# Kernel optimization log

Measured on AMD Instinct MI355X. Metric: run time of the kernel, lower is better.

Reference implementation:

```python
import jax, jax.numpy as jnp
import numpy as np
import math

B, TQ, TK, C, H, DFF = 4, 1024, 1024, 1024, 16, 4096
DK = C // H
EPS = 1e-12


def _mha(x_q, x_kv, wq, bq, wk, bk, wv, bv, wo, bo, mask):
    Bq, Tq, Cq = x_q.shape
    Tk = x_kv.shape[1]
    q = (x_q @ wq + bq).reshape(Bq, Tq, H, DK).transpose(0, 2, 1, 3)  # [B,H,Tq,dk]
    k = (x_kv @ wk + bk).reshape(Bq, Tk, H, DK).transpose(0, 2, 1, 3)
    v = (x_kv @ wv + bv).reshape(Bq, Tk, H, DK).transpose(0, 2, 1, 3)
    scores = jnp.einsum('bhqd,bhkd->bhqk', q, k) * (1.0 / math.sqrt(DK))
    if mask is not None:
        scores = jnp.where(mask, scores, jnp.asarray(-1e9, scores.dtype))
    attn = jax.nn.softmax(scores, axis=-1)
    o = jnp.einsum('bhqk,bhkd->bhqd', attn, v).transpose(0, 2, 1, 3).reshape(Bq, Tq, Cq)
    return o @ wo + bo


def _ln(x, g, b):
    mu = jnp.mean(x, axis=-1, keepdims=True)
    var = jnp.mean(jnp.square(x - mu), axis=-1, keepdims=True)
    return (x - mu) * jax.lax.rsqrt(var + EPS) * g + b


def setup_inputs() -> dict:
    key = jax.random.key(0)
    ks = iter(jax.random.split(key, 32))
    s = 0.02
    inp = {}
    inp['src'] = jax.random.normal(next(ks), (B, TK, C), jnp.float32)
    inp['dst'] = jax.random.normal(next(ks), (B, TQ, C), jnp.float32)
    inp['src_mask'] = jnp.ones((B, 1, 1, TK), dtype=bool)  # key-padding mask (all valid)
    inp['dst_mask'] = jnp.tril(jnp.ones((TQ, TQ), dtype=bool))[None, None]  # causal
    for p in ['sa', 'ca']:
        for n in ['wq', 'wk', 'wv', 'wo']:
            inp[f'{p}_{n}'] = jax.random.normal(next(ks), (C, C), jnp.float32) * s
        for n in ['bq', 'bk', 'bv', 'bo']:
            inp[f'{p}_{n}'] = jnp.zeros((C,), jnp.float32)
    inp['ffn_w1'] = jax.random.normal(next(ks), (C, DFF), jnp.float32) * s
    inp['ffn_b1'] = jnp.zeros((DFF,), jnp.float32)
    inp['ffn_w2'] = jax.random.normal(next(ks), (DFF, C), jnp.float32) * s
    inp['ffn_b2'] = jnp.zeros((C,), jnp.float32)
    for i in ['1', '2', '3']:
        inp[f'ln{i}_g'] = jnp.ones((C,), jnp.float32)
        inp[f'ln{i}_b'] = jnp.zeros((C,), jnp.float32)
    return inp


def reference(src, dst, src_mask, dst_mask,
              sa_wq, sa_wk, sa_wv, sa_wo, sa_bq, sa_bk, sa_bv, sa_bo,
              ca_wq, ca_wk, ca_wv, ca_wo, ca_bq, ca_bk, ca_bv, ca_bo,
              ffn_w1, ffn_b1, ffn_w2, ffn_b2,
              ln1_g, ln1_b, ln2_g, ln2_b, ln3_g, ln3_b):
    # post-LN decoder layer, eval mode (dropout is identity)
    sa = _mha(dst, dst, sa_wq, sa_bq, sa_wk, sa_bk, sa_wv, sa_bv, sa_wo, sa_bo, dst_mask)
    y = _ln(dst + sa, ln1_g, ln1_b)
    ca = _mha(y, src, ca_wq, ca_bq, ca_wk, ca_bk, ca_wv, ca_bv, ca_wo, ca_bo, src_mask)
    y = _ln(y + ca, ln2_g, ln2_b)
    ff = jax.nn.gelu(y @ ffn_w1 + ffn_b1, approximate=False) @ ffn_w2 + ffn_b2
    return _ln(y + ff, ln3_g, ln3_b)
```

## Files before the change

### kernel.cpp

```cpp
#include <hip/hip_runtime.h>
#include <math.h>

typedef __attribute__((ext_vector_type(4))) float f32x4;
typedef __attribute__((ext_vector_type(8))) __bf16 bf16x8;
typedef __attribute__((ext_vector_type(8))) short short8;

#define DEV __device__ __forceinline__

DEV short f2bfs(float f) {
    unsigned u = __builtin_bit_cast(unsigned, f);
    unsigned r = (u + 0x7FFFu + ((u >> 16) & 1u)) >> 16;
    return (short)r;
}

DEV f32x4 mfma16(bf16x8 a, bf16x8 b, f32x4 c) {
    return __builtin_amdgcn_mfma_f32_16x16x32_bf16(a, b, c, 0, 0, 0);
}

DEV void gload_lds16(const void* g, void* l) {
    __builtin_amdgcn_global_load_lds((const __attribute__((address_space(1))) void*)g,
                                     (__attribute__((address_space(3))) void*)l, 16, 0, 0);
}

__global__ __launch_bounds__(256) void wtrans(const float* __restrict__ Win,
                                              short* __restrict__ Wout,
                                              int Kd, int Nd) {
    __shared__ float Tt[32][33];
    const int tx = threadIdx.x & 31, ty = threadIdx.x >> 5;
    const int k0 = blockIdx.y * 32, n0 = blockIdx.x * 32;
#pragma unroll
    for (int rr = 0; rr < 4; ++rr) {
        int k = ty * 4 + rr;
        Tt[k][tx] = Win[(size_t)(k0 + k) * Nd + n0 + tx];
    }
    __syncthreads();
#pragma unroll
    for (int rr = 0; rr < 4; ++rr) {
        int n = ty * 4 + rr;
        Wout[(size_t)(n0 + n) * Kd + k0 + tx] = f2bfs(Tt[tx][n]);
    }
}

struct WPtrs { const float* p[8]; };

__global__ __launch_bounds__(256) void wtrans8(WPtrs wp, short* __restrict__ out) {
    const float* __restrict__ Win = wp.p[blockIdx.z];
    short* __restrict__ Wout = out + (size_t)blockIdx.z * (1024 * 1024);
    __shared__ float Tt[32][33];
    const int tx = threadIdx.x & 31, ty = threadIdx.x >> 5;
    const int k0 = blockIdx.y * 32, n0 = blockIdx.x * 32;
#pragma unroll
    for (int rr = 0; rr < 4; ++rr) {
        int k = ty * 4 + rr;
        Tt[k][tx] = Win[(size_t)(k0 + k) * 1024 + n0 + tx];
    }
    __syncthreads();
#pragma unroll
    for (int rr = 0; rr < 4; ++rr) {
        int n = ty * 4 + rr;
        Wout[(size_t)(n0 + n) * 1024 + k0 + tx] = f2bfs(Tt[tx][n]);
    }
}

__global__ __launch_bounds__(256) void conv_bf16(const float* __restrict__ X,
                                                 short* __restrict__ Y, int n4) {
    int i = blockIdx.x * 256 + threadIdx.x;
    if (i < n4) {
        float4 v = ((const float4*)X)[i];
        short4 o;
        o.x = f2bfs(v.x); o.y = f2bfs(v.y); o.z = f2bfs(v.z); o.w = f2bfs(v.w);
        ((short4*)Y)[i] = o;
    }
}

template <int BM, int BN, int EPI, bool SWZ>
__global__ __launch_bounds__(256, (BM == 64 && BN == 64) ? 8 : 1)
void gemm_bt(const short* __restrict__ A,
             const short* __restrict__ BT,
             const float* __restrict__ b0,
             const float* __restrict__ b1,
             const float* __restrict__ b2,
             void* __restrict__ o0,
             void* __restrict__ o1,
             void* __restrict__ o2,
             int M, int N, int K, int Ks) {
    constexpr int IM = BM / 32, JN = BN / 32;
    constexpr int AL = (BM * 64) / 4096;
    constexpr int BL = (BN * 64) / 4096;
    __shared__ __align__(16) short As[2][BM * 32];
    __shared__ __align__(16) short Bs[2][128 * 32];
    const int tid = threadIdx.x, lane = tid & 63, w = tid >> 6;

    int bx, by, bz;
    if (SWZ) {
        int gx = gridDim.x, gy = gridDim.y;
        int G = gx * gy * gridDim.z;
        int fid = blockIdx.x + gx * (blockIdx.y + gy * blockIdx.z);
        int nf = (fid & 7) * (G >> 3) + (fid >> 3);
        bx = nf % gx;
        int t = nf / gx;
        by = t % gy;
        bz = t / gy;
    } else {
        bx = blockIdx.x; by = blockIdx.y; bz = blockIdx.z;
    }

    const int m0 = by * BM, n0 = bx * BN;
    const int kz = bz * K;
    const int wm = (w & 1) * (BM / 2), wn = (w >> 1) * (BN / 2);
    const int rl = lane & 15, rg = lane >> 4;
    f32x4 acc[IM][JN] = {};
    const char* Ab = (const char*)A;
    const char* Bb = (const char*)BT;
    const int nk = K >> 5;

    auto stage = [&](int kt, int buf) {
#pragma unroll
        for (int r = 0; r < AL; ++r) {
            int lo = (tid + r * 256) * 16;
            int row = lo >> 6, cp = (lo >> 4) & 3, c = (cp - (row >> 1)) & 3;
            gload_lds16(Ab + ((size_t)(m0 + row) * Ks + kz + kt * 32 + c * 8) * 2,
                        (char*)As[buf] + lo);
        }
#pragma unroll
        for (int r = 0; r < BL; ++r) {
            int lo = (tid + r * 256) * 16;
            int row = lo >> 6, cp = (lo >> 4) & 3, c = (cp - (row >> 1)) & 3;
            gload_lds16(Bb + ((size_t)(n0 + row) * Ks + kz + kt * 32 + c * 8) * 2,
                        (char*)Bs[buf] + lo);
        }
    };

    stage(0, 0);
    for (int kt = 0; kt < nk; ++kt) {
        const int buf = kt & 1;
        __syncthreads();
        if (kt + 1 < nk) stage(kt + 1, buf ^ 1);
        bf16x8 af[IM], bfr[JN];
#pragma unroll
        for (int i = 0; i < IM; i++) {
            int row = wm + i * 16 + rl;
            af[i] = *(const bf16x8*)(As[buf] + row * 32 + ((rg + (row >> 1)) & 3) * 8);
        }
#pragma unroll
        for (int j = 0; j < JN; j++) {
            int row = wn + j * 16 + rl;
            bfr[j] = *(const bf16x8*)(Bs[buf] + row * 32 + ((rg + (row >> 1)) & 3) * 8);
        }
#pragma unroll
        for (int i = 0; i < IM; i++)
#pragma unroll
            for (int j = 0; j < JN; j++)
                acc[i][j] = mfma16(af[i], bfr[j], acc[i][j]);
    }

    float* o0z = (float*)o0 + (size_t)bz * M * N;
#pragma unroll
    for (int i = 0; i < IM; i++) {
        int gm0 = m0 + wm + i * 16 + rg * 4;
#pragma unroll
        for (int j = 0; j < JN; j++) {
            int gn = n0 + wn + j * 16 + rl;
            if (EPI == 0) {
                float bv = bz == 0 ? b0[gn] : 0.0f;
#pragma unroll
                for (int r = 0; r < 4; r++)
                    o0z[(size_t)(gm0 + r) * N + gn] = acc[i][j][r] + bv;
            } else if (EPI == 2) {
                float bv = b0[gn];
#pragma unroll
                for (int r = 0; r < 4; r++) {
                    float x = acc[i][j][r] + bv;
                    float z = 1.59576912f * x + 0.07135481f * x * x * x;
                    float g = x / (1.0f + __expf(-z));
                    ((short*)o0)[(size_t)(gm0 + r) * N + gn] = f2bfs(g);
                }
            } else {
                int seg = gn >> 10, n1 = gn & 1023, h = n1 >> 6, d = n1 & 63;
                int b = gm0 >> 10, t0 = gm0 & 1023;
                bool isV = (EPI == 1) ? (seg == 2) : (seg == 1);
                const float* bp = (EPI == 1) ? (seg == 0 ? b0 : (seg == 1 ? b1 : b2))
                                             : (seg == 0 ? b0 : b1);
                float bv = bp[n1];
                float qs = (EPI == 1 && seg == 0) ? 0.125f : 1.0f;
                if (!isV) {
                    short* hp = (short*)((EPI == 1) ? (seg == 0 ? o0 : o1) : o0);
                    size_t base = ((size_t)(b * 16 + h) * 1024 + t0) * 64 + d;
#pragma unroll
                    for (int r = 0; r < 4; r++)
                        hp[base + (size_t)r * 64] = f2bfs((acc[i][j][r] + bv) * qs);
                } else {
                    short* vp = (short*)((EPI == 1) ? o2 : o1);
                    short4 pk;
                    pk.x = f2bfs(acc[i][j][0] + bv);
                    pk.y = f2bfs(acc[i][j][1] + bv);
                    pk.z = f2bfs(acc[i][j][2] + bv);
                    pk.w = f2bfs(acc[i][j][3] + bv);
                    *(short4*)(vp + ((size_t)(b * 16 + h) * 64 + d) * 1024 + t0) = pk;
                }
            }
        }
    }
}

template <bool CAUSAL>
__global__ __launch_bounds__(256, 3) void attn4(const short* __restrict__ Qh,
                                                const short* __restrict__ Kh,
                                                const short* __restrict__ VTh,
                                                short* __restrict__ Out, int TKn) {
    __shared__ __align__(16) short Ks[2][64 * 64];
    __shared__ __align__(16) short Vts[2][64 * 64];
    __shared__ __align__(16) short Ps[4][16 * 72 + 8];
    const int tid = threadIdx.x, lane = tid & 63, w = tid >> 6;
    const int rl = lane & 15, rg = lane >> 4;
    const int bh = blockIdx.y, b = bh >> 4, h = bh & 15;
    const int q0 = blockIdx.x * 64;
    const short* Qp = Qh + (size_t)bh * 1024 * 64;
    const char* Kp = (const char*)(Kh + (size_t)bh * (size_t)TKn * 64);
    const char* Vp = (const char*)(VTh + (size_t)bh * (size_t)TKn * 64);

    const int qrow = q0 + w * 16 + rl;
    const bf16x8 qf0 = *(const bf16x8*)(Qp + (size_t)qrow * 64 + rg * 8);
    const bf16x8 qf1 = *(const bf16x8*)(Qp + (size_t)qrow * 64 + 32 + rg * 8);

    bf16x8 onesf;
#pragma unroll
    for (int i = 0; i < 8; ++i) onesf[i] = (__bf16)1.0f;

    f32x4 o[4] = {};
    f32x4 lacc = {};

    short* Pw = &Ps[w][0];
    const int nkt = CAUSAL ? blockIdx.x + 1 : (TKn >> 6);

    auto stage = [&](int kt, int buf) {
#pragma unroll
        for (int r = 0; r < 2; ++r) {
            int lo = (w * 2 + r) * 1024 + lane * 16;
            int row = lo >> 7, cp = (lo >> 4) & 7, c = (cp - row) & 7;
            gload_lds16(Kp + ((size_t)(kt * 64 + row) * 64 + c * 8) * 2,
                        (char*)Ks[buf] + lo);
            gload_lds16(Vp + ((size_t)row * TKn + kt * 64 + c * 8) * 2,
                        (char*)Vts[buf] + lo);
        }
    };

    stage(0, 0);
    for (int kt = 0; kt < nkt; ++kt) {
        const int buf = kt & 1;
        __syncthreads();
        if (kt + 1 < nkt) stage(kt + 1, buf ^ 1);

        const short* KsB = Ks[buf];
        f32x4 s[4];
#pragma unroll
        for (int ch = 0; ch < 4; ++ch) {
            int row = ch * 16 + rl;
            bf16x8 k0 = *(const bf16x8*)(KsB + row * 64 + ((rg + row) & 7) * 8);
            bf16x8 k1 = *(const bf16x8*)(KsB + row * 64 + ((rg + 4 + row) & 7) * 8);
            f32x4 z = {};
            z = mfma16(k0, qf0, z);
            z = mfma16(k1, qf1, z);
            s[ch] = z;
        }
        const bool domask = CAUSAL && (kt == nkt - 1);
#pragma unroll
        for (int ch = 0; ch < 4; ++ch) {
            float p[4];
#pragma unroll
            for (int r = 0; r < 4; ++r) {
                float e = __expf(s[ch][r]);
                if (domask) {
                    int key = kt * 64 + ch * 16 + rg * 4 + r;
                    if (key > qrow) e = 0.0f;
                }
                p[r] = e;
            }
            unsigned d0 = (__builtin_bit_cast(unsigned, p[1]) & 0xFFFF0000u) |
                          (__builtin_bit_cast(unsigned, p[0]) >> 16);
            unsigned d1 = (__builtin_bit_cast(unsigned, p[3]) & 0xFFFF0000u) |
                          (__builtin_bit_cast(unsigned, p[2]) >> 16);
            uint2 dv; dv.x = d0; dv.y = d1;
            *(uint2*)(Pw + rl * 72 + ch * 16 + rg * 4) = dv;
        }
        bf16x8 pa0 = *(const bf16x8*)(Pw + rl * 72 + rg * 8);
        bf16x8 pa1 = *(const bf16x8*)(Pw + rl * 72 + 32 + rg * 8);
        lacc = mfma16(pa0, onesf, lacc);
        lacc = mfma16(pa1, onesf, lacc);
        const short* VsB = Vts[buf];
#pragma unroll
        for (int j = 0; j < 4; ++j) {
            int row = j * 16 + rl;
            bf16x8 v0 = *(const bf16x8*)(VsB + row * 64 + ((rg + row) & 7) * 8);
            bf16x8 v1 = *(const bf16x8*)(VsB + row * 64 + ((rg + 4 + row) & 7) * 8);
            o[j] = mfma16(pa0, v0, o[j]);
            o[j] = mfma16(pa1, v1, o[j]);
        }
    }

    float inv[4];
#pragma unroll
    for (int r = 0; r < 4; r++) inv[r] = 1.0f / lacc[r];
#pragma unroll
    for (int j = 0; j < 4; j++) {
#pragma unroll
        for (int r = 0; r < 4; r++) {
            int row = q0 + w * 16 + rg * 4 + r;
            int col = h * 64 + j * 16 + rl;
            Out[((size_t)b * 1024 + row) * 1024 + col] = f2bfs(o[j][r] * inv[r]);
        }
    }
}

__global__ __launch_bounds__(256) void ln_fused(const float* __restrict__ X,
                                                const float* __restrict__ R,
                                                const float* __restrict__ R2,
                                                const float* __restrict__ gam,
                                                const float* __restrict__ bet,
                                                float* __restrict__ Yf,
                                                short* __restrict__ Yb) {
    const int row = blockIdx.x, tid = threadIdx.x;
    const int lane = tid & 63, w = tid >> 6;
    float4 xv = ((const float4*)(X + (size_t)row * 1024))[tid];
    float4 rv = ((const float4*)(R + (size_t)row * 1024))[tid];
    float v0 = xv.x + rv.x, v1 = xv.y + rv.y, v2 = xv.z + rv.z, v3 = xv.w + rv.w;
    if (R2) {
        float4 r2 = ((const float4*)(R2 + (size_t)row * 1024))[tid];
        v0 += r2.x; v1 += r2.y; v2 += r2.z; v3 += r2.w;
    }
    float s = v0 + v1 + v2 + v3;
    float ss = v0 * v0 + v1 * v1 + v2 * v2 + v3 * v3;
#pragma unroll
    for (int off = 1; off < 64; off <<= 1) {
        s += __shfl_xor(s, off);
        ss += __shfl_xor(ss, off);
    }
    __shared__ float sred[4], ssred[4];
    if (lane == 0) { sred[w] = s; ssred[w] = ss; }
    __syncthreads();
    s = sred[0] + sred[1] + sred[2] + sred[3];
    ss = ssred[0] + ssred[1] + ssred[2] + ssred[3];
    float mu = s * (1.0f / 1024.0f);
    float var = ss * (1.0f / 1024.0f) - mu * mu;
    float rsq = rsqrtf(var + 1e-12f);
    float4 gv = ((const float4*)gam)[tid];
    float4 bv = ((const float4*)bet)[tid];
    float y0 = (v0 - mu) * rsq * gv.x + bv.x;
    float y1 = (v1 - mu) * rsq * gv.y + bv.y;
    float y2 = (v2 - mu) * rsq * gv.z + bv.z;
    float y3 = (v3 - mu) * rsq * gv.w + bv.w;
    float4 yo = {y0, y1, y2, y3};
    ((float4*)(Yf + (size_t)row * 1024))[tid] = yo;
    if (Yb) {
        short4 ob;
        ob.x = f2bfs(y0); ob.y = f2bfs(y1); ob.z = f2bfs(y2); ob.w = f2bfs(y3);
        ((short4*)(Yb + (size_t)row * 1024))[tid] = ob;
    }
}

extern "C" void kernel_launch(void* const* d_in, const int* in_sizes, int n_in,
                              void* d_out, int out_size, void* d_ws, size_t ws_size,
                              hipStream_t stream) {
    const float* src = (const float*)d_in[0];
    const float* dst = (const float*)d_in[1];
    const float* sa_wq = (const float*)d_in[4];
    const float* sa_wk = (const float*)d_in[5];
    const float* sa_wv = (const float*)d_in[6];
    const float* sa_wo = (const float*)d_in[7];
    const float* sa_bq = (const float*)d_in[8];
    const float* sa_bk = (const float*)d_in[9];
    const float* sa_bv = (const float*)d_in[10];
    const float* sa_bo = (const float*)d_in[11];
    const float* ca_wq = (const float*)d_in[12];
    const float* ca_wk = (const float*)d_in[13];
    const float* ca_wv = (const float*)d_in[14];
    const float* ca_wo = (const float*)d_in[15];
    const float* ca_bq = (const float*)d_in[16];
    const float* ca_bk = (const float*)d_in[17];
    const float* ca_bv = (const float*)d_in[18];
    const float* ca_bo = (const float*)d_in[19];
    const float* ffn_w1 = (const float*)d_in[20];
    const float* ffn_b1 = (const float*)d_in[21];
    const float* ffn_w2 = (const float*)d_in[22];
    const float* ffn_b2 = (const float*)d_in[23];
    const float* ln1g = (const float*)d_in[24];
    const float* ln1b = (const float*)d_in[25];
    const float* ln2g = (const float*)d_in[26];
    const float* ln2b = (const float*)d_in[27];
    const float* ln3g = (const float*)d_in[28];
    const float* ln3b = (const float*)d_in[29];

    char* ws = (char*)d_ws;
    size_t off = 0;
    auto alloc = [&](size_t n) { size_t o = off; off = (off + n + 255) & ~(size_t)255; return o; };

    const size_t szW = (size_t)1024 * 1024 * 2;
    short* wT = (short*)(ws + alloc(8 * szW));
    short* w1T = (short*)(ws + alloc((size_t)4096 * 1024 * 2));
    short* w2T = (short*)(ws + alloc((size_t)1024 * 4096 * 2));
    const size_t szAct2 = (size_t)4096 * 1024 * 2;
    const size_t szAct4 = (size_t)4096 * 1024 * 4;
    short* dstb = (short*)(ws + alloc(szAct2));
    short* srcb = (short*)(ws + alloc(szAct2));
    short* Qh = (short*)(ws + alloc(szAct2));
    short* Kh = (short*)(ws + alloc(szAct2));
    short* VTh = (short*)(ws + alloc(szAct2));
    short* attnb = (short*)(ws + alloc(szAct2));
    float* tmp = (float*)(ws + alloc(2 * szAct4));
    float* tmp2 = tmp + (size_t)4096 * 1024;
    float* y1f = (float*)(ws + alloc(szAct4));
    short* y1b = (short*)(ws + alloc(szAct2));
    float* y2f = (float*)(ws + alloc(szAct4));
    short* y2b = (short*)(ws + alloc(szAct2));
    short* ffnh = (short*)(ws + alloc((size_t)4096 * 4096 * 2));

    short* sa_wqkvT = wT;
    short* sa_woT = wT + 3 * (size_t)1048576;
    short* ca_wqT = wT + 4 * (size_t)1048576;
    short* ca_wkvT = wT + 5 * (size_t)1048576;
    short* ca_woT = wT + 7 * (size_t)1048576;

    dim3 blk(256);

    WPtrs wp = {{sa_wq, sa_wk, sa_wv, sa_wo, ca_wq, ca_wk, ca_wv, ca_wo}};
    wtrans8<<<dim3(32, 32, 8), blk, 0, stream>>>(wp, wT);
    wtrans<<<dim3(128, 32), blk, 0, stream>>>(ffn_w1, w1T, 1024, 4096);
    wtrans<<<dim3(32, 128), blk, 0, stream>>>(ffn_w2, w2T, 4096, 1024);
    conv_bf16<<<4096, blk, 0, stream>>>(dst, dstb, 1048576);
    conv_bf16<<<4096, blk, 0, stream>>>(src, srcb, 1048576);

    gemm_bt<128, 128, 1, false><<<dim3(24, 32), blk, 0, stream>>>(
        dstb, sa_wqkvT, sa_bq, sa_bk, sa_bv, Qh, Kh, VTh, 4096, 3072, 1024, 1024);
    attn4<true><<<dim3(16, 64), blk, 0, stream>>>(Qh, Kh, VTh, attnb, 1024);
    gemm_bt<64, 64, 0, true><<<dim3(16, 64, 2), blk, 0, stream>>>(
        attnb, sa_woT, sa_bo, nullptr, nullptr, tmp, nullptr, nullptr, 4096, 1024, 512, 1024);
    ln_fused<<<4096, blk, 0, stream>>>(dst, tmp, tmp2, ln1g, ln1b, y1f, y1b);

    gemm_bt<64, 64, 1, true><<<dim3(16, 64), blk, 0, stream>>>(
        y1b, ca_wqT, ca_bq, nullptr, nullptr, Qh, nullptr, nullptr, 4096, 1024, 1024, 1024);
    gemm_bt<128, 128, 3, false><<<dim3(16, 32), blk, 0, stream>>>(
        srcb, ca_wkvT, ca_bk, ca_bv, nullptr, Kh, VTh, nullptr, 4096, 2048, 1024, 1024);
    attn4<false><<<dim3(16, 64), blk, 0, stream>>>(Qh, Kh, VTh, attnb, 1024);
    gemm_bt<64, 64, 0, true><<<dim3(16, 64, 2), blk, 0, stream>>>(
        attnb, ca_woT, ca_bo, nullptr, nullptr, tmp, nullptr, nullptr, 4096, 1024, 512, 1024);
    ln_fused<<<4096, blk, 0, stream>>>(y1f, tmp, tmp2, ln2g, ln2b, y2f, y2b);

    gemm_bt<128, 128, 2, false><<<dim3(32, 32), blk, 0, stream>>>(
        y2b, w1T, ffn_b1, nullptr, nullptr, ffnh, nullptr, nullptr, 4096, 4096, 1024, 1024);
    gemm_bt<64, 64, 0, true><<<dim3(16, 64, 2), blk, 0, stream>>>(
        ffnh, w2T, ffn_b2, nullptr, nullptr, tmp, nullptr, nullptr, 4096, 1024, 2048, 4096);
    ln_fused<<<4096, blk, 0, stream>>>(y2f, tmp, tmp2, ln3g, ln3b, (float*)d_out, nullptr);

    (void)in_sizes; (void)n_in; (void)out_size; (void)ws_size;
}
```

Before: 546.4 us.

## Triple-buffer LDS staging with partial vmcnt waits in 64x64 GEMM tiles

```diff
diff --git a/kernel.cpp b/kernel.cpp
--- a/kernel.cpp
+++ b/kernel.cpp
@@ -74,7 +74,7 @@
 }
 
 template <int BM, int BN, int EPI, bool SWZ>
-__global__ __launch_bounds__(256, (BM == 64 && BN == 64) ? 8 : 1)
+__global__ __launch_bounds__(256, (BM == 64 && BN == 64) ? 6 : 1)
 void gemm_bt(const short* __restrict__ A,
              const short* __restrict__ BT,
              const float* __restrict__ b0,
@@ -87,8 +87,10 @@
     constexpr int IM = BM / 32, JN = BN / 32;
     constexpr int AL = (BM * 64) / 4096;
     constexpr int BL = (BN * 64) / 4096;
-    __shared__ __align__(16) short As[2][BM * 32];
-    __shared__ __align__(16) short Bs[2][128 * 32];
+    constexpr bool PIPE = (BM == 64 && BN == 64);
+    constexpr int NB = PIPE ? 3 : 2;
+    __shared__ __align__(16) short As[NB][BM * 32];
+    __shared__ __align__(16) short Bs[NB][BN * 32];
     const int tid = threadIdx.x, lane = tid & 63, w = tid >> 6;
 
     int bx, by, bz;
@@ -131,27 +133,61 @@
         }
     };
 
-    stage(0, 0);
-    for (int kt = 0; kt < nk; ++kt) {
-        const int buf = kt & 1;
-        __syncthreads();
-        if (kt + 1 < nk) stage(kt + 1, buf ^ 1);
-        bf16x8 af[IM], bfr[JN];
-#pragma unroll
-        for (int i = 0; i < IM; i++) {
-            int row = wm + i * 16 + rl;
-            af[i] = *(const bf16x8*)(As[buf] + row * 32 + ((rg + (row >> 1)) & 3) * 8);
-        }
-#pragma unroll
-        for (int j = 0; j < JN; j++) {
-            int row = wn + j * 16 + rl;
-            bfr[j] = *(const bf16x8*)(Bs[buf] + row * 32 + ((rg + (row >> 1)) & 3) * 8);
-        }
-#pragma unroll
-        for (int i = 0; i < IM; i++)
-#pragma unroll
-            for (int j = 0; j < JN; j++)
-                acc[i][j] = mfma16(af[i], bfr[j], acc[i][j]);
+    if constexpr (PIPE) {
+        stage(0, 0);
+        if (nk > 1) stage(1, 1);
+        int buf = 0;
+        for (int kt = 0; kt < nk; ++kt) {
+            if (kt + 1 < nk)
+                asm volatile("s_waitcnt vmcnt(2)" ::: "memory");
+            else
+                asm volatile("s_waitcnt vmcnt(0)" ::: "memory");
+            __builtin_amdgcn_s_barrier();
+            if (kt + 2 < nk) {
+                int bs = buf + 2; if (bs >= 3) bs -= 3;
+                stage(kt + 2, bs);
+            }
+            bf16x8 af[IM], bfr[JN];
+#pragma unroll
+            for (int i = 0; i < IM; i++) {
+                int row = wm + i * 16 + rl;
+                af[i] = *(const bf16x8*)(As[buf] + row * 32 + ((rg + (row >> 1)) & 3) * 8);
+            }
+#pragma unroll
+            for (int j = 0; j < JN; j++) {
+                int row = wn + j * 16 + rl;
+                bfr[j] = *(const bf16x8*)(Bs[buf] + row * 32 + ((rg + (row >> 1)) & 3) * 8);
+            }
+#pragma unroll
+            for (int i = 0; i < IM; i++)
+#pragma unroll
+                for (int j = 0; j < JN; j++)
+                    acc[i][j] = mfma16(af[i], bfr[j], acc[i][j]);
+            buf = (buf == 2) ? 0 : buf + 1;
+        }
+    } else {
+        stage(0, 0);
+        for (int kt = 0; kt < nk; ++kt) {
+            const int buf = kt & 1;
+            __syncthreads();
+            if (kt + 1 < nk) stage(kt + 1, buf ^ 1);
+            bf16x8 af[IM], bfr[JN];
+#pragma unroll
+            for (int i = 0; i < IM; i++) {
+                int row = wm + i * 16 + rl;
+                af[i] = *(const bf16x8*)(As[buf] + row * 32 + ((rg + (row >> 1)) & 3) * 8);
+            }
+#pragma unroll
+            for (int j = 0; j < JN; j++) {
+                int row = wn + j * 16 + rl;
+                bfr[j] = *(const bf16x8*)(Bs[buf] + row * 32 + ((rg + (row >> 1)) & 3) * 8);
+            }
+#pragma unroll
+            for (int i = 0; i < IM; i++)
+#pragma unroll
+                for (int j = 0; j < JN; j++)
+                    acc[i][j] = mfma16(af[i], bfr[j], acc[i][j]);
+        }
     }
 
     float* o0z = (float*)o0 + (size_t)bz * M * N;
```

Measured after the change: 544.2 us. No clear change (-0.4%).

## Deepen K tile to 64 and drop split-K for 64x64 output GEMMs

Applied to the files above, without the earlier changes.

```diff
diff --git a/kernel.cpp b/kernel.cpp
--- a/kernel.cpp
+++ b/kernel.cpp
@@ -73,8 +73,8 @@
     }
 }
 
-template <int BM, int BN, int EPI, bool SWZ>
-__global__ __launch_bounds__(256, (BM == 64 && BN == 64) ? 8 : 1)
+template <int BM, int BN, int BK, int EPI, bool SWZ>
+__global__ __launch_bounds__(256, (BM == 64 && BN == 64) ? 4 : 1)
 void gemm_bt(const short* __restrict__ A,
              const short* __restrict__ BT,
              const float* __restrict__ b0,
@@ -85,10 +85,11 @@
              void* __restrict__ o2,
              int M, int N, int K, int Ks) {
     constexpr int IM = BM / 32, JN = BN / 32;
+    constexpr int KH = BK / 32;
     constexpr int AL = (BM * 64) / 4096;
     constexpr int BL = (BN * 64) / 4096;
-    __shared__ __align__(16) short As[2][BM * 32];
-    __shared__ __align__(16) short Bs[2][128 * 32];
+    __shared__ __align__(16) short As[2][BM * BK];
+    __shared__ __align__(16) short Bs[2][BN * BK];
     const int tid = threadIdx.x, lane = tid & 63, w = tid >> 6;
 
     int bx, by, bz;
@@ -112,22 +113,25 @@
     f32x4 acc[IM][JN] = {};
     const char* Ab = (const char*)A;
     const char* Bb = (const char*)BT;
-    const int nk = K >> 5;
+    const int nk = K / BK;
 
     auto stage = [&](int kt, int buf) {
 #pragma unroll
-        for (int r = 0; r < AL; ++r) {
-            int lo = (tid + r * 256) * 16;
-            int row = lo >> 6, cp = (lo >> 4) & 3, c = (cp - (row >> 1)) & 3;
-            gload_lds16(Ab + ((size_t)(m0 + row) * Ks + kz + kt * 32 + c * 8) * 2,
-                        (char*)As[buf] + lo);
-        }
-#pragma unroll
-        for (int r = 0; r < BL; ++r) {
-            int lo = (tid + r * 256) * 16;
-            int row = lo >> 6, cp = (lo >> 4) & 3, c = (cp - (row >> 1)) & 3;
-            gload_lds16(Bb + ((size_t)(n0 + row) * Ks + kz + kt * 32 + c * 8) * 2,
-                        (char*)Bs[buf] + lo);
+        for (int h = 0; h < KH; ++h) {
+#pragma unroll
+            for (int r = 0; r < AL; ++r) {
+                int lo = (tid + r * 256) * 16;
+                int row = lo >> 6, cp = (lo >> 4) & 3, c = (cp - (row >> 1)) & 3;
+                gload_lds16(Ab + ((size_t)(m0 + row) * Ks + kz + kt * BK + h * 32 + c * 8) * 2,
+                            (char*)As[buf] + h * (BM * 64) + lo);
+            }
+#pragma unroll
+            for (int r = 0; r < BL; ++r) {
+                int lo = (tid + r * 256) * 16;
+                int row = lo >> 6, cp = (lo >> 4) & 3, c = (cp - (row >> 1)) & 3;
+                gload_lds16(Bb + ((size_t)(n0 + row) * Ks + kz + kt * BK + h * 32 + c * 8) * 2,
+                            (char*)Bs[buf] + h * (BN * 64) + lo);
+            }
         }
     };
 
@@ -136,22 +140,29 @@
         const int buf = kt & 1;
         __syncthreads();
         if (kt + 1 < nk) stage(kt + 1, buf ^ 1);
-        bf16x8 af[IM], bfr[JN];
-#pragma unroll
-        for (int i = 0; i < IM; i++) {
-            int row = wm + i * 16 + rl;
-            af[i] = *(const bf16x8*)(As[buf] + row * 32 + ((rg + (row >> 1)) & 3) * 8);
-        }
-#pragma unroll
-        for (int j = 0; j < JN; j++) {
-            int row = wn + j * 16 + rl;
-            bfr[j] = *(const bf16x8*)(Bs[buf] + row * 32 + ((rg + (row >> 1)) & 3) * 8);
-        }
-#pragma unroll
-        for (int i = 0; i < IM; i++)
-#pragma unroll
-            for (int j = 0; j < JN; j++)
-                acc[i][j] = mfma16(af[i], bfr[j], acc[i][j]);
+        bf16x8 af[KH][IM], bfr[KH][JN];
+#pragma unroll
+        for (int h = 0; h < KH; ++h) {
+#pragma unroll
+            for (int i = 0; i < IM; i++) {
+                int row = wm + i * 16 + rl;
+                af[h][i] = *(const bf16x8*)(As[buf] + h * (BM * 32) + row * 32 +
+                                            ((rg + (row >> 1)) & 3) * 8);
+            }
+#pragma unroll
+            for (int j = 0; j < JN; j++) {
+                int row = wn + j * 16 + rl;
+                bfr[h][j] = *(const bf16x8*)(Bs[buf] + h * (BN * 32) + row * 32 +
+                                             ((rg + (row >> 1)) & 3) * 8);
+            }
+        }
+#pragma unroll
+        for (int h = 0; h < KH; ++h)
+#pragma unroll
+            for (int i = 0; i < IM; i++)
+#pragma unroll
+                for (int j = 0; j < JN; j++)
+                    acc[i][j] = mfma16(af[h][i], bfr[h][j], acc[i][j]);
     }
 
     float* o0z = (float*)o0 + (size_t)bz * M * N;
@@ -406,8 +417,7 @@
     short* Kh = (short*)(ws + alloc(szAct2));
     short* VTh = (short*)(ws + alloc(szAct2));
     short* attnb = (short*)(ws + alloc(szAct2));
-    float* tmp = (float*)(ws + alloc(2 * szAct4));
-    float* tmp2 = tmp + (size_t)4096 * 1024;
+    float* tmp = (float*)(ws + alloc(szAct4));
     float* y1f = (float*)(ws + alloc(szAct4));
     short* y1b = (short*)(ws + alloc(szAct2));
     float* y2f = (float*)(ws + alloc(szAct4));
@@ -429,27 +439,27 @@
     conv_bf16<<<4096, blk, 0, stream>>>(dst, dstb, 1048576);
     conv_bf16<<<4096, blk, 0, stream>>>(src, srcb, 1048576);
 
-    gemm_bt<128, 128, 1, false><<<dim3(24, 32), blk, 0, stream>>>(
+    gemm_bt<128, 128, 32, 1, false><<<dim3(24, 32), blk, 0, stream>>>(
         dstb, sa_wqkvT, sa_bq, sa_bk, sa_bv, Qh, Kh, VTh, 4096, 3072, 1024, 1024);
     attn4<true><<<dim3(16, 64), blk, 0, stream>>>(Qh, Kh, VTh, attnb, 1024);
-    gemm_bt<64, 64, 0, true><<<dim3(16, 64, 2), blk, 0, stream>>>(
-        attnb, sa_woT, sa_bo, nullptr, nullptr, tmp, nullptr, nullptr, 4096, 1024, 512, 1024);
-    ln_fused<<<4096, blk, 0, stream>>>(dst, tmp, tmp2, ln1g, ln1b, y1f, y1b);
-
-    gemm_bt<64, 64, 1, true><<<dim3(16, 64), blk, 0, stream>>>(
+    gemm_bt<64, 64, 64, 0, true><<<dim3(16, 64), blk, 0, stream>>>(
+        attnb, sa_woT, sa_bo, nullptr, nullptr, tmp, nullptr, nullptr, 4096, 1024, 1024, 1024);
+    ln_fused<<<4096, blk, 0, stream>>>(dst, tmp, nullptr, ln1g, ln1b, y1f, y1b);
+
+    gemm_bt<64, 64, 64, 1, true><<<dim3(16, 64), blk, 0, stream>>>(
         y1b, ca_wqT, ca_bq, nullptr, nullptr, Qh, nullptr, nullptr, 4096, 1024, 1024, 1024);
-    gemm_bt<128, 128, 3, false><<<dim3(16, 32), blk, 0, stream>>>(
+    gemm_bt<128, 128, 32, 3, false><<<dim3(16, 32), blk, 0, stream>>>(
         srcb, ca_wkvT, ca_bk, ca_bv, nullptr, Kh, VTh, nullptr, 4096, 2048, 1024, 1024);
     attn4<false><<<dim3(16, 64), blk, 0, stream>>>(Qh, Kh, VTh, attnb, 1024);
-    gemm_bt<64, 64, 0, true><<<dim3(16, 64, 2), blk, 0, stream>>>(
-        attnb, ca_woT, ca_bo, nullptr, nullptr, tmp, nullptr, nullptr, 4096, 1024, 512, 1024);
-    ln_fused<<<4096, blk, 0, stream>>>(y1f, tmp, tmp2, ln2g, ln2b, y2f, y2b);
-
-    gemm_bt<128, 128, 2, false><<<dim3(32, 32), blk, 0, stream>>>(
+    gemm_bt<64, 64, 64, 0, true><<<dim3(16, 64), blk, 0, stream>>>(
+        attnb, ca_woT, ca_bo, nullptr, nullptr, tmp, nullptr, nullptr, 4096, 1024, 1024, 1024);
+    ln_fused<<<4096, blk, 0, stream>>>(y1f, tmp, nullptr, ln2g, ln2b, y2f, y2b);
+
+    gemm_bt<128, 128, 32, 2, false><<<dim3(32, 32), blk, 0, stream>>>(
         y2b, w1T, ffn_b1, nullptr, nullptr, ffnh, nullptr, nullptr, 4096, 4096, 1024, 1024);
-    gemm_bt<64, 64, 0, true><<<dim3(16, 64, 2), blk, 0, stream>>>(
-        ffnh, w2T, ffn_b2, nullptr, nullptr, tmp, nullptr, nullptr, 4096, 1024, 2048, 4096);
-    ln_fused<<<4096, blk, 0, stream>>>(y2f, tmp, tmp2, ln3g, ln3b, (float*)d_out, nullptr);
+    gemm_bt<64, 64, 64, 0, true><<<dim3(16, 64), blk, 0, stream>>>(
+        ffnh, w2T, ffn_b2, nullptr, nullptr, tmp, nullptr, nullptr, 4096, 1024, 4096, 4096);
+    ln_fused<<<4096, blk, 0, stream>>>(y2f, tmp, nullptr, ln3g, ln3b, (float*)d_out, nullptr);
 
     (void)in_sizes; (void)n_in; (void)out_size; (void)ws_size;
 }
```

Result: faster. 515.5 us (-5.7%).
